# Performance work log

Hardware: AMD Instinct MI355X
Metric: run time of the kernel (lower is better)

Reference implementation:

```python
import jax, jax.numpy as jnp
import numpy as np

BS, N_STK, N_STK_PNT = 4, 32, 128
N_PNT = N_STK * N_STK_PNT
SP_IN, DN_IN = 128, 128
SP_OUT, DN_OUT = 256, 256
SP_NEAR, DN_NEAR = 2, 10
COOR = 128


def _conv2d(x, w, b, stride=(1, 1), pad='VALID'):
    # x [bs,C,H,W], w [O,I,kh,kw]
    y = jax.lax.conv_general_dilated(x, w, window_strides=stride, padding=pad,
                                     dimension_numbers=('NCHW', 'OIHW', 'NCHW'))
    return y + b[None, :, None, None]


def _fps(xyz, n_sample):
    # farthest point sampling. xyz [bs,n,c] -> [bs,n_sample] int32
    n = xyz.shape[1]

    def one(x):
        def body(i, state):
            idx, dist, far = state
            idx = idx.at[i].set(far)
            d = jnp.sum((x - x[far]) ** 2, axis=-1)
            dist = jnp.minimum(dist, d)
            return idx, dist, jnp.argmax(dist).astype(jnp.int32)

        idx0 = jnp.zeros((n_sample,), jnp.int32)
        dist0 = jnp.full((n,), 1e10, x.dtype)
        idx, _, _ = jax.lax.fori_loop(0, n_sample, body, (idx0, dist0, jnp.int32(0)))
        return idx

    return jax.vmap(one)(xyz)


def _gcn(x, W, b, g, bt, k):
    # DGCNN edge-conv. x [bs,c,n]; W [2c,co]
    xt = jnp.swapaxes(x, 1, 2)                                   # [bs,n,c]
    sq = jnp.sum(xt * xt, axis=-1)                               # [bs,n]
    dist = sq[:, :, None] - 2.0 * jnp.einsum('bnc,bmc->bnm', xt, xt) + sq[:, None, :]
    _, idx = jax.lax.top_k(-dist, k)                             # [bs,n,k]
    nbr = jax.vmap(lambda p, i: p[i])(xt, idx)                   # [bs,n,k,c]
    ctr = jnp.broadcast_to(xt[:, :, None, :], nbr.shape)
    edge = jnp.concatenate([ctr, nbr - ctr], axis=-1)            # [bs,n,k,2c]
    h = jnp.einsum('bnke,eo->bnko', edge, W) + b
    h = jax.nn.relu(g * h + bt)
    return jnp.swapaxes(jnp.max(h, axis=2), 1, 2)                # [bs,co,n]


def setup_inputs() -> dict:
    key = jax.random.key(0)
    ks = jax.random.split(key, 16)
    f32 = jnp.float32
    d = {
        'sparse_fea': jax.random.normal(ks[0], (BS, SP_IN, N_STK), f32),
        'dense_fea': jax.random.normal(ks[1], (BS, DN_IN, N_PNT), f32),
        'stk_coor': jax.random.normal(ks[2], (BS, N_STK, COOR), f32),
        # DenseToSparse: Conv2d(dn_in->dn_in, (1,3)) + BN
        'd2s_w': jax.random.normal(ks[3], (DN_IN, DN_IN, 1, 3), f32) * 0.05,
        'd2s_b': jnp.zeros((DN_IN,), f32),
        'd2s_g': jnp.ones((DN_IN,), f32),
        'd2s_bt': jnp.zeros((DN_IN,), f32),
        # sparse GCN: in = SP_IN + DN_IN, edge feat 2*in
        'sp_W': jax.random.normal(ks[4], (2 * (SP_IN + DN_IN), SP_OUT), f32) * 0.05,
        'sp_b': jnp.zeros((SP_OUT,), f32),
        'sp_g': jnp.ones((SP_OUT,), f32),
        'sp_bt': jnp.zeros((SP_OUT,), f32),
        # dense GCN: in = DN_IN + SP_IN
        'dn_W': jax.random.normal(ks[5], (2 * (DN_IN + SP_IN), DN_OUT), f32) * 0.05,
        'dn_b': jnp.zeros((DN_OUT,), f32),
        'dn_g': jnp.ones((DN_OUT,), f32),
        'dn_bt': jnp.zeros((DN_OUT,), f32),
        # DownSample: Conv2d(dn_out->dn_out, (1,3), stride (1,2), pad (0,1)) + BN
        'ds_w': jax.random.normal(ks[6], (DN_OUT, DN_OUT, 1, 3), f32) * 0.05,
        'ds_b': jnp.zeros((DN_OUT,), f32),
        'ds_g': jnp.ones((DN_OUT,), f32),
        'ds_bt': jnp.zeros((DN_OUT,), f32),
    }
    return d


def reference(sparse_fea, dense_fea, stk_coor,
              d2s_w, d2s_b, d2s_g, d2s_bt,
              sp_W, sp_b, sp_g, sp_bt,
              dn_W, dn_b, dn_g, dn_bt,
              ds_w, ds_b, ds_g, ds_bt):
    bs = sparse_fea.shape[0]
    df = dense_fea.reshape(bs, DN_IN, N_STK, N_STK_PNT)
    # DenseToSparse: conv (1,3) valid + BN(eval) + relu + max over stroke points
    h = _conv2d(df, d2s_w, d2s_b)
    h = jax.nn.relu(d2s_g[None, :, None, None] * h + d2s_bt[None, :, None, None])
    sp_from_dn = jnp.max(h, axis=3)                                    # [bs,dn_in,n_stk]
    union_sparse = jnp.concatenate([sparse_fea, sp_from_dn], axis=1)   # [bs,sp_in+dn_in,n_stk]
    # SparseToDense: broadcast stroke feature onto its points
    dn_from_sp = jnp.broadcast_to(sparse_fea[:, :, :, None], (bs, SP_IN, N_STK, N_STK_PNT))
    union_dense = jnp.concatenate([df, dn_from_sp], axis=1).reshape(bs, DN_IN + SP_IN, N_PNT)
    # GCN (DGCNN edge conv) updates
    sparse_up = _gcn(union_sparse, sp_W, sp_b, sp_g, sp_bt, SP_NEAR)   # [bs,SP_OUT,n_stk]
    dense_up = _gcn(union_dense, dn_W, dn_b, dn_g, dn_bt, DN_NEAR)     # [bs,DN_OUT,n_pnt]
    # DownSample: FPS on stroke coords, gather strokes, strided conv on points
    n_half = N_STK // 2
    fps_idx = _fps(stk_coor, n_half)                                   # [bs,n_half]
    stk_coor_s = jnp.take_along_axis(stk_coor, fps_idx[:, :, None], axis=1)
    sp_s = jnp.take_along_axis(jnp.swapaxes(sparse_up, 1, 2), fps_idx[:, :, None], axis=1)
    sp_s = jnp.swapaxes(sp_s, 1, 2)                                    # [bs,SP_OUT,n_half]
    dn = dense_up.reshape(bs, DN_OUT, N_STK, N_STK_PNT)
    dn = jnp.take_along_axis(dn, fps_idx[:, None, :, None], axis=2)    # [bs,DN_OUT,n_half,n_stk_pnt]
    dn = _conv2d(dn, ds_w, ds_b, stride=(1, 2), pad=[(0, 0), (1, 1)])
    dn = jax.nn.relu(ds_g[None, :, None, None] * dn + ds_bt[None, :, None, None])
    dn = dn.reshape(bs, DN_OUT, n_half * (N_STK_PNT // 2))
    return sp_s, dn, stk_coor_s
```

## Files before the change

kernel.cpp:

```cpp
#include <hip/hip_runtime.h>

#define NPNT 4096
#define NSTK 32

typedef _Float16 half8 __attribute__((ext_vector_type(8)));
typedef float f32x4 __attribute__((ext_vector_type(4)));
typedef unsigned long long u64;

static const size_t OFF_XT   = 0;
static const size_t OFF_P    = 4194304;
static const size_t OFF_Q    = 8388608;
static const size_t OFF_SQD  = 12582912;
static const size_t OFF_SPFD = 12599296;
static const size_t OFF_XS   = 12615680;
static const size_t OFF_PS   = 12648448;
static const size_t OFF_QS   = 12681216;
static const size_t OFF_WSP  = 12746752;
static const size_t OFF_KNN  = 13402112;
static const size_t OFF_IDXS = 13565952;
static const size_t OFF_FPS  = 13566208;
static const size_t OFF_SD   = 13566272;

__device__ __forceinline__ void insertK(u64 lk[10], u64 k) {
  if (k >= lk[9]) return;
  lk[9] = k;
#pragma unroll
  for (int j = 9; j > 0; j--) {
    u64 a = lk[j-1], b2 = lk[j];
    bool sw = b2 < a;
    lk[j-1] = sw ? b2 : a;
    lk[j]   = sw ? a : b2;
  }
}

#define CASK(a, b) { u64 _x = (a), _y = (b); bool _s = _y < _x; \
  (a) = _s ? _y : _x; (b) = _s ? _x : _y; }

__device__ __forceinline__ void merge10(u64 lk[10], const u64 b[10]) {
  u64 c[10];
#pragma unroll
  for (int i = 0; i < 10; i++) { u64 t = b[9 - i]; u64 a = lk[i]; c[i] = a < t ? a : t; }
  CASK(c[0], c[5]); CASK(c[1], c[6]); CASK(c[2], c[7]); CASK(c[3], c[8]); CASK(c[4], c[9]);
  CASK(c[0], c[1]); CASK(c[1], c[2]); CASK(c[2], c[3]); CASK(c[3], c[4]);
  CASK(c[0], c[1]); CASK(c[1], c[2]); CASK(c[2], c[3]);
  CASK(c[0], c[1]); CASK(c[1], c[2]);
  CASK(c[0], c[1]);
  CASK(c[5], c[6]); CASK(c[6], c[7]); CASK(c[7], c[8]); CASK(c[8], c[9]);
  CASK(c[5], c[6]); CASK(c[6], c[7]); CASK(c[7], c[8]);
  CASK(c[5], c[6]); CASK(c[6], c[7]);
  CASK(c[5], c[6]);
#pragma unroll
  for (int i = 0; i < 10; i++) lk[i] = c[i];
}

__global__ __launch_bounds__(256) void k_pre(
    const float* __restrict__ df, const float* __restrict__ sf,
    const float* __restrict__ coor, const float* __restrict__ dnW,
    const float* __restrict__ d2sw, const float* __restrict__ d2scb,
    const float* __restrict__ d2sg, const float* __restrict__ d2sbt,
    _Float16* __restrict__ XH, _Float16* __restrict__ XL, float* __restrict__ sqd,
    _Float16* __restrict__ WPh, _Float16* __restrict__ WPl,
    _Float16* __restrict__ WQh, _Float16* __restrict__ WQl,
    float* __restrict__ spfd, int* __restrict__ fpsidx, float* __restrict__ out2) {
  __shared__ __align__(16) char SMEM[46080];
  const int bid = blockIdx.x;
  const int t = threadIdx.x;

  if (bid < 4) {
    int b = bid;
    float (*X)[132] = (float (*)[132])SMEM;
    float* dist = (float*)(SMEM + 16896);
    int* far_s  = (int*)(SMEM + 17024);
    int* sel    = (int*)(SMEM + 17028);
    for (int idx = t; idx < 32 * 32; idx += 256) {
      int r = idx >> 5, q = idx & 31;
      *(float4*)&X[r][q * 4] = *(const float4*)&coor[((size_t)b * 32 + r) * 128 + q * 4];
    }
    if (t < 32) dist[t] = 1e10f;
    if (t == 0) *far_s = 0;
    __syncthreads();
    for (int it = 0; it < 16; it++) {
      int far = *far_s;
      if (t == 0) sel[it] = far;
      if (t < 32) {
        float d = 0.0f;
        for (int c = 0; c < 128; c++) { float dd = X[t][c] - X[far][c]; d = fmaf(dd, dd, d); }
        float dm = dist[t];
        dist[t] = d < dm ? d : dm;
      }
      __syncthreads();
      if (t == 0) {
        float best = -1.0f; int bi = 0;
        for (int m = 0; m < 32; m++) if (dist[m] > best) { best = dist[m]; bi = m; }
        *far_s = bi;
      }
      __syncthreads();
    }
    if (t < 16) fpsidx[b * 16 + t] = sel[t];
    __syncthreads();
    for (int idx = t; idx < 16 * 32; idx += 256) {
      int j = idx >> 5, q = idx & 31;
      *(float4*)&out2[((size_t)b * 16 + j) * 128 + q * 4] = *(const float4*)&X[sel[j]][q * 4];
    }
  } else if (bid < 260) {
    int idx0 = bid - 4;
    int b = idx0 & 3, n0 = (idx0 >> 2) * 64;
    int s0 = n0 >> 7;
    float (*T)[68] = (float (*)[68])SMEM;
    _Float16* Sh = (_Float16*)(SMEM + 34816);
    _Float16* Sl = (_Float16*)(SMEM + 35072);
    {
      int c = t >> 1, nh = (t & 1) * 32;
      const float* src = &df[((size_t)b * 128 + c) * NPNT + n0 + nh];
#pragma unroll
      for (int j = 0; j < 8; j++) *(float4*)&T[c][nh + j * 4] = *(const float4*)&src[j * 4];
    }
    if (t < 128) {
      float x = sf[((size_t)b * 128 + t) * NSTK + s0];
      _Float16 hi = (_Float16)x;
      Sh[t] = hi; Sl[t] = (_Float16)(x - (float)hi);
    }
    __syncthreads();
    {
      int n = t >> 2, cseg = (t & 3) * 32;
      size_t base = ((size_t)b * NPNT + n0 + n) * 256;
      float s = 0.0f;
#pragma unroll
      for (int k = 0; k < 4; k++) {
        half8 hv, lv, shv, slv;
#pragma unroll
        for (int e = 0; e < 8; e++) {
          float x = T[cseg + k * 8 + e][n];
          s = fmaf(x, x, s);
          _Float16 hi = (_Float16)x;
          hv[e] = hi; lv[e] = (_Float16)(x - (float)hi);
          shv[e] = Sh[cseg + k * 8 + e];
          slv[e] = Sl[cseg + k * 8 + e];
        }
        *(half8*)&XH[base + cseg + k * 8] = hv;
        *(half8*)&XL[base + cseg + k * 8] = lv;
        *(half8*)&XH[base + 128 + cseg + k * 8] = shv;
        *(half8*)&XL[base + 128 + cseg + k * 8] = slv;
      }
      s += __shfl_xor(s, 1);
      s += __shfl_xor(s, 2);
      if ((t & 3) == 0) sqd[(size_t)b * NPNT + n0 + n] = s;
    }
  } else if (bid < 516) {
    int idx0 = bid - 260;
    int b = idx0 & 3, o0 = ((idx0 >> 2) & 1) * 64, s = idx0 >> 3;
    int n0 = s * 128;
    float (*A)[64]   = (float (*)[64])SMEM;
    float (*Bs)[132] = (float (*)[132])(SMEM + 24576);
    float (*Dr)[17]  = (float (*)[17])(SMEM + 41472);
    float acc[4][8];
#pragma unroll
    for (int i = 0; i < 4; i++)
#pragma unroll
      for (int j = 0; j < 8; j++) acc[i][j] = 0.0f;
    int tn = t & 15, to = t >> 4;
    for (int ic = 0; ic < 128; ic += 32) {
      {
        int ol = t >> 2, q = t & 3;
        const float* src = &d2sw[((size_t)(o0 + ol) * 128 + ic) * 3 + q * 24];
#pragma unroll
        for (int r = 0; r < 6; r++) {
          float4 v = *(const float4*)&src[r * 4];
          int e = q * 24 + r * 4;
          A[e+0][ol] = v.x; A[e+1][ol] = v.y; A[e+2][ol] = v.z; A[e+3][ol] = v.w;
        }
      }
      for (int idx = t; idx < 32 * 33; idx += 256) {
        int row = idx / 33, f4 = idx % 33;
        int nb = n0 + f4 * 4;
        const float* srow = &df[((size_t)b * 128 + ic + row) * NPNT];
        float4 v;
        if (nb + 3 < NPNT) v = *(const float4*)&srow[nb];
        else {
          v.x = srow[nb   < NPNT ? nb   : NPNT-1];
          v.y = srow[nb+1 < NPNT ? nb+1 : NPNT-1];
          v.z = srow[nb+2 < NPNT ? nb+2 : NPNT-1];
          v.w = srow[nb+3 < NPNT ? nb+3 : NPNT-1];
        }
        *(float4*)&Bs[row][f4 * 4] = v;
      }
      __syncthreads();
#pragma unroll 2
      for (int ii = 0; ii < 32; ii++) {
        float bv[12];
        *(float4*)&bv[0] = *(const float4*)&Bs[ii][tn * 8];
        *(float4*)&bv[4] = *(const float4*)&Bs[ii][tn * 8 + 4];
        *(float4*)&bv[8] = *(const float4*)&Bs[ii][tn * 8 + 8];
#pragma unroll
        for (int kw = 0; kw < 3; kw++) {
          float4 av = *(const float4*)&A[ii * 3 + kw][to * 4];
#pragma unroll
          for (int j = 0; j < 8; j++) {
            float bvj = bv[kw + j];
            acc[0][j] = fmaf(av.x, bvj, acc[0][j]);
            acc[1][j] = fmaf(av.y, bvj, acc[1][j]);
            acc[2][j] = fmaf(av.z, bvj, acc[2][j]);
            acc[3][j] = fmaf(av.w, bvj, acc[3][j]);
          }
        }
      }
      __syncthreads();
    }
#pragma unroll
    for (int i = 0; i < 4; i++) {
      int o = o0 + to * 4 + i;
      float gg = d2sg[o], bb = d2scb[o], bo = d2sbt[o];
      float m = 0.0f;
#pragma unroll
      for (int j = 0; j < 8; j++) {
        int p = tn * 8 + j;
        if (p < 126) {
          float v = fmaf(gg, acc[i][j] + bb, bo);
          v = v > 0.0f ? v : 0.0f;
          m = v > m ? v : m;
        }
      }
      Dr[to * 4 + i][tn] = m;
    }
    __syncthreads();
    if (t < 64) {
      float m = 0.0f;
#pragma unroll
      for (int k = 0; k < 16; k++) m = Dr[t][k] > m ? Dr[t][k] : m;
      spfd[((size_t)b * 128 + o0 + t) * NSTK + s] = m;
    }
  } else {
    int k = bid - 516, o = t;
    float w1 = dnW[(size_t)k * 256 + o];
    float w2 = dnW[(size_t)(k + 256) * 256 + o];
    float p = w1 - w2;
    _Float16 ph = (_Float16)p;  WPh[(size_t)o * 256 + k] = ph;
    WPl[(size_t)o * 256 + k] = (_Float16)(p - (float)ph);
    _Float16 qh = (_Float16)w2; WQh[(size_t)o * 256 + k] = qh;
    WQl[(size_t)o * 256 + k] = (_Float16)(w2 - (float)qh);
  }
}

__global__ __launch_bounds__(256) void k_sparse_graph(const float* __restrict__ sf, const float* __restrict__ spfd,
    float* __restrict__ xs, int* __restrict__ idxs, float* __restrict__ SD) {
  int b = blockIdx.x, t = threadIdx.x;
  __shared__ float X[32][260];
  __shared__ float sq[32];
  __shared__ float D[32][33];
  for (int idx = t; idx < 32 * 256; idx += 256) {
    int n = idx >> 8, c = idx & 255;
    float v = (c < 128) ? sf[((size_t)b * 128 + c) * NSTK + n]
                        : spfd[((size_t)b * 128 + (c - 128)) * NSTK + n];
    X[n][c] = v;
  }
  __syncthreads();
  for (int idx = t; idx < 32 * 64; idx += 256) {
    int n = idx >> 6, q = idx & 63;
    *(float4*)&xs[((size_t)b * 32 + n) * 256 + q * 4] = *(const float4*)&X[n][q * 4];
  }
#pragma unroll
  for (int rep = 0; rep < 4; rep++) {
    int p = t + rep * 256;
    int s = p >> 5, u = p & 31;
    float acc = 0.0f;
    for (int c = 0; c < 128; c++) {
      float d = X[s][c] - X[u][c];
      acc = fmaf(d, d, acc);
    }
    SD[(size_t)b * 1024 + p] = acc;
  }
  if (t < 32) {
    float s = 0.0f;
    for (int c = 0; c < 256; c++) s = fmaf(X[t][c], X[t][c], s);
    sq[t] = s;
  }
  __syncthreads();
  {
    int n = t >> 3;
    for (int mg = 0; mg < 4; mg++) {
      int m = (t & 7) + mg * 8;
      float dot = 0.0f;
      for (int c = 0; c < 256; c++) dot = fmaf(X[n][c], X[m][c], dot);
      D[n][m] = (sq[n] - 2.0f * dot) + sq[m];
    }
  }
  __syncthreads();
  if (t < 32) {
    float d0 = 1e30f, d1 = 1e30f; int i0 = 0, i1 = 0;
    for (int m = 0; m < 32; m++) {
      float d = D[t][m];
      if (d < d0) { d1 = d0; i1 = i0; d0 = d; i0 = m; }
      else if (d < d1) { d1 = d; i1 = m; }
    }
    idxs[(b * 32 + t) * 2 + 0] = i0;
    idxs[(b * 32 + t) * 2 + 1] = i1;
  }
}

__global__ __launch_bounds__(256) void k_sparse_pq(const float* __restrict__ xs, const float* __restrict__ W,
    float* __restrict__ Ps, float* __restrict__ Qs) {
  int b = blockIdx.x >> 5, n = blockIdx.x & 31;
  int o = threadIdx.x;
  const float* xr = &xs[((size_t)b * 32 + n) * 256];
  float accP = 0.0f, accQ = 0.0f;
  for (int c = 0; c < 256; c++) {
    float xc = xr[c];
    float w1 = W[(size_t)c * 256 + o];
    float w2 = W[(size_t)(c + 256) * 256 + o];
    accP = fmaf(xc, w1 - w2, accP);
    accQ = fmaf(xc, w2, accQ);
  }
  Ps[((size_t)b * 32 + n) * 256 + o] = accP;
  Qs[((size_t)b * 32 + n) * 256 + o] = accQ;
}

__global__ __launch_bounds__(256) void k_sparse_cg(const float* __restrict__ Ps, const float* __restrict__ Qs,
    const int* __restrict__ idxs, const int* __restrict__ fps,
    const float* __restrict__ g, const float* __restrict__ cb, const float* __restrict__ bt,
    float* __restrict__ out0) {
  int b = blockIdx.x, j = blockIdx.y, o = threadIdx.x;
  int n = fps[b * 16 + j];
  int i0 = idxs[(b * 32 + n) * 2 + 0], i1 = idxs[(b * 32 + n) * 2 + 1];
  float p = Ps[((size_t)b * 32 + n) * 256 + o];
  float q0 = Qs[((size_t)b * 32 + i0) * 256 + o];
  float q1 = Qs[((size_t)b * 32 + i1) * 256 + o];
  float gg = g[o], bb = cb[o], bo = bt[o];
  float h0 = fmaf(gg, p + q0 + bb, bo); h0 = h0 > 0.0f ? h0 : 0.0f;
  float h1 = fmaf(gg, p + q1 + bb, bo); h1 = h1 > 0.0f ? h1 : 0.0f;
  out0[((size_t)b * 256 + o) * 16 + j] = h0 > h1 ? h0 : h1;
}

#define STAGE(ch2_, p_) { \
  int srow = t >> 2, scol = (t & 3) * 16; \
  size_t gp = (bofs + (size_t)(m0 + (ch2_) * 64 + srow)) * 256 + (p_) * 64 + scol; \
  float4 gh0 = *(const float4*)&XH[gp]; float4 gh1 = *(const float4*)&XH[gp + 8]; \
  float4 gl0 = *(const float4*)&XL[gp]; float4 gl1 = *(const float4*)&XL[gp + 8]; \
  int lo = srow * 72 + scol; \
  *(float4*)&BshH[lo] = gh0; *(float4*)&BshH[lo + 8] = gh1; \
  *(float4*)&BshL[lo] = gl0; *(float4*)&BshL[lo + 8] = gl1; }

#define DWU(wv_, r_, c_) DwU[(((wv_) * 16 + (r_)) * 68) + (c_)]

__global__ __launch_bounds__(256, 4) void k_knn_mfma(const _Float16* __restrict__ XH,
    const _Float16* __restrict__ XL, const float* __restrict__ sqd, const float* __restrict__ SD,
    const int* __restrict__ fps, u64* __restrict__ pk) {
  const int h = blockIdx.x, rb = blockIdx.y, b = blockIdx.z;
  const int t = threadIdx.x;
  const int w = t >> 6, L = t & 63;
  const int c15 = L & 15, q = L >> 4;
  const int jst = rb >> 1;
  const int ph = (rb & 1) * 64;
  const int s_stk = fps[b * 16 + jst];
  const int nsrc = s_stk * 128 + ph + w * 16;
  const int rc0 = rb * 64 + w * 16;
  const size_t bofs = (size_t)b * NPNT;

  __shared__ __align__(16) char SMEM[18432];
  _Float16* const BshH = (_Float16*)SMEM;
  _Float16* const BshL = (_Float16*)(SMEM + 64 * 72 * 2);
  unsigned* const DwU = (unsigned*)SMEM;

  half8 ah[4], al[4];
  {
    const _Float16* ap  = XH + (bofs + nsrc + c15) * 256 + q * 8;
    const _Float16* apl = XL + (bofs + nsrc + c15) * 256 + q * 8;
#pragma unroll
    for (int ch = 0; ch < 4; ch++) {
      ah[ch] = *(const half8*)(ap + ch * 32);
      al[ch] = *(const half8*)(apl + ch * 32);
    }
  }
  float snr[4];
#pragma unroll
  for (int r = 0; r < 4; r++) snr[r] = sqd[bofs + nsrc + q * 4 + r];

  u64 lk[10];
#pragma unroll
  for (int j = 0; j < 10; j++) lk[j] = ~0ull;

  const bool own_here = ((s_stk >> 1) == h);
  const int r_sel = L >> 2, sl = L & 3;
  const int u0 = own_here ? s_stk : (h * 2);
  const int u1 = own_here ? (s_stk ^ 1) : (h * 2 + 1);

#pragma unroll 1
  for (int it = 0; it < 2; it++) {
    const int u = (it == 0) ? u0 : u1;
    const int m0 = u * 128;
    const float SDv = SD[((size_t)b * 32 + s_stk) * 32 + u];

#pragma unroll 1
    for (int ch2 = 0; ch2 < 2; ch2++) {
      float smv[4];
#pragma unroll
      for (int cg = 0; cg < 4; cg++) smv[cg] = sqd[bofs + m0 + ch2 * 64 + cg * 16 + c15];

      f32x4 zz = {0.0f, 0.0f, 0.0f, 0.0f};
      f32x4 acc[4];
#pragma unroll
      for (int cg = 0; cg < 4; cg++) acc[cg] = zz;

      __syncthreads();
      STAGE(ch2, 0);
      __syncthreads();
#pragma unroll
      for (int chl = 0; chl < 2; chl++) {
#pragma unroll
        for (int cg = 0; cg < 4; cg++) {
          int lo = (cg * 16 + c15) * 72 + chl * 32 + q * 8;
          half8 bh = *(const half8*)&BshH[lo];
          half8 bl = *(const half8*)&BshL[lo];
          acc[cg] = __builtin_amdgcn_mfma_f32_16x16x32_f16(ah[chl], bh, acc[cg], 0, 0, 0);
          acc[cg] = __builtin_amdgcn_mfma_f32_16x16x32_f16(ah[chl], bl, acc[cg], 0, 0, 0);
          acc[cg] = __builtin_amdgcn_mfma_f32_16x16x32_f16(al[chl], bh, acc[cg], 0, 0, 0);
        }
      }
      __syncthreads();
      STAGE(ch2, 1);
      __syncthreads();
#pragma unroll
      for (int chl = 0; chl < 2; chl++) {
#pragma unroll
        for (int cg = 0; cg < 4; cg++) {
          int lo = (cg * 16 + c15) * 72 + chl * 32 + q * 8;
          half8 bh = *(const half8*)&BshH[lo];
          half8 bl = *(const half8*)&BshL[lo];
          acc[cg] = __builtin_amdgcn_mfma_f32_16x16x32_f16(ah[2 + chl], bh, acc[cg], 0, 0, 0);
          acc[cg] = __builtin_amdgcn_mfma_f32_16x16x32_f16(ah[2 + chl], bl, acc[cg], 0, 0, 0);
          acc[cg] = __builtin_amdgcn_mfma_f32_16x16x32_f16(al[2 + chl], bh, acc[cg], 0, 0, 0);
        }
      }
      __syncthreads();

#pragma unroll
      for (int cg = 0; cg < 4; cg++) {
        float basec = SDv + smv[cg];
#pragma unroll
        for (int r = 0; r < 4; r++) {
          float d = fmaf(-2.0f, acc[cg][r], snr[r] + basec);
          unsigned uu = __float_as_uint(d);
          unsigned kk = uu ^ ((unsigned)((int)uu >> 31) | 0x80000000u);
          DWU(w, q * 4 + r, cg * 16 + c15) = kk;
        }
      }
#pragma unroll
      for (int jj = 0; jj < 4; jj++) {
        uint4 kv = *(const uint4*)&DWU(w, r_sel, jj * 16 + sl * 4);
        int ib = m0 + ch2 * 64 + jj * 16 + sl * 4;
        insertK(lk, ((u64)kv.x << 32) | (unsigned)(ib + 0));
        insertK(lk, ((u64)kv.y << 32) | (unsigned)(ib + 1));
        insertK(lk, ((u64)kv.z << 32) | (unsigned)(ib + 2));
        insertK(lk, ((u64)kv.w << 32) | (unsigned)(ib + 3));
      }
    }
  }

#pragma unroll
  for (int m = 1; m <= 2; m <<= 1) {
    u64 o[10];
#pragma unroll
    for (int j = 0; j < 10; j++) o[j] = __shfl_xor(lk[j], m);
    merge10(lk, o);
  }
  if (sl == 0) {
    size_t row = (size_t)b * 2048 + rc0 + r_sel;
    u64* dst = &pk[(row * 16 + h) * 10];
#pragma unroll
    for (int j = 0; j < 10; j++) dst[j] = lk[j];
  }
}

__global__ __launch_bounds__(256) void k_knn_merge(const u64* __restrict__ pk,
                                                   int* __restrict__ knnc) {
  int gid = blockIdx.x * 256 + threadIdx.x;
  size_t row = (size_t)(gid >> 2);
  int sl = gid & 3;
  const u64* src = &pk[row * 160 + (size_t)sl * 40];
  u64 lk[10];
#pragma unroll
  for (int j = 0; j < 10; j++) lk[j] = src[j];
#pragma unroll
  for (int l = 1; l < 4; l++) {
    u64 bv[10];
#pragma unroll
    for (int j = 0; j < 10; j++) bv[j] = src[l * 10 + j];
    merge10(lk, bv);
  }
#pragma unroll
  for (int m = 1; m <= 2; m <<= 1) {
    u64 o[10];
#pragma unroll
    for (int j = 0; j < 10; j++) o[j] = __shfl_xor(lk[j], m);
    merge10(lk, o);
  }
  if (sl == 0) {
#pragma unroll
    for (int j = 0; j < 10; j++) knnc[row * 10 + j] = (int)(unsigned)(lk[j] & 0xffffffffull);
  }
}

__global__ __launch_bounds__(256, 2) void k_pq_mfma(const _Float16* __restrict__ XH, const _Float16* __restrict__ XL,
    const _Float16* __restrict__ WPh, const _Float16* __restrict__ WPl,
    const _Float16* __restrict__ WQh, const _Float16* __restrict__ WQl,
    const int* __restrict__ fps, const float* __restrict__ g, const float* __restrict__ cb,
    const float* __restrict__ bt, float* __restrict__ Pc, float* __restrict__ Qp) {
  const int b = blockIdx.z;
  const int t = threadIdx.x, w = t >> 6, L = t & 63;
  const int c15 = L & 15, q = L >> 4;
  const int ow = blockIdx.y * 128 + (w >> 1) * 64;
  const size_t bofs = (size_t)b * NPNT;
  f32x4 zz = {0.0f, 0.0f, 0.0f, 0.0f};

  {
    const int nw = blockIdx.x * 32 + (w & 1) * 16;
    f32x4 accQ[4];
#pragma unroll
    for (int cg = 0; cg < 4; cg++) accQ[cg] = zz;
    const _Float16* ap  = XH + (bofs + nw + c15) * 256 + q * 8;
    const _Float16* apl = XL + (bofs + nw + c15) * 256 + q * 8;
#pragma unroll
    for (int ch = 0; ch < 8; ch++) {
      half8 a_h = *(const half8*)(ap + ch * 32);
      half8 a_l = *(const half8*)(apl + ch * 32);
#pragma unroll
      for (int cg = 0; cg < 4; cg++) {
        size_t wb = (size_t)(ow + cg * 16 + c15) * 256 + ch * 32 + q * 8;
        half8 bqh = *(const half8*)(WQh + wb);
        half8 bql = *(const half8*)(WQl + wb);
        accQ[cg] = __builtin_amdgcn_mfma_f32_16x16x32_f16(a_h, bqh, accQ[cg], 0, 0, 0);
        accQ[cg] = __builtin_amdgcn_mfma_f32_16x16x32_f16(a_h, bql, accQ[cg], 0, 0, 0);
        accQ[cg] = __builtin_amdgcn_mfma_f32_16x16x32_f16(a_l, bqh, accQ[cg], 0, 0, 0);
      }
    }
#pragma unroll
    for (int cg = 0; cg < 4; cg++) {
      int o = ow + cg * 16 + c15;
      float gg = g[o];
#pragma unroll
      for (int r = 0; r < 4; r++) {
        Qp[(bofs + nw + q * 4 + r) * 256 + o] = gg * accQ[cg][r];
      }
    }
  }

  if (blockIdx.x < 64) {
    const int m0 = blockIdx.x * 32 + (w & 1) * 16;
    const int jst = m0 >> 7;
    const int pbase = m0 & 127;
    const int nsrc = fps[b * 16 + jst] * 128 + pbase;
    f32x4 accP[4];
#pragma unroll
    for (int cg = 0; cg < 4; cg++) accP[cg] = zz;
    const _Float16* ap  = XH + (bofs + nsrc + c15) * 256 + q * 8;
    const _Float16* apl = XL + (bofs + nsrc + c15) * 256 + q * 8;
#pragma unroll
    for (int ch = 0; ch < 8; ch++) {
      half8 a_h = *(const half8*)(ap + ch * 32);
      half8 a_l = *(const half8*)(apl + ch * 32);
#pragma unroll
      for (int cg = 0; cg < 4; cg++) {
        size_t wb = (size_t)(ow + cg * 16 + c15) * 256 + ch * 32 + q * 8;
        half8 bph = *(const half8*)(WPh + wb);
        half8 bpl = *(const half8*)(WPl + wb);
        accP[cg] = __builtin_amdgcn_mfma_f32_16x16x32_f16(a_h, bph, accP[cg], 0, 0, 0);
        accP[cg] = __builtin_amdgcn_mfma_f32_16x16x32_f16(a_h, bpl, accP[cg], 0, 0, 0);
        accP[cg] = __builtin_amdgcn_mfma_f32_16x16x32_f16(a_l, bph, accP[cg], 0, 0, 0);
      }
    }
#pragma unroll
    for (int cg = 0; cg < 4; cg++) {
      int o = ow + cg * 16 + c15;
      float gg = g[o], bb = cb[o], bo = bt[o];
#pragma unroll
      for (int r = 0; r < 4; r++) {
        Pc[(((size_t)b * 16 + jst) * 128 + pbase + q * 4 + r) * 256 + o] =
            fmaf(gg, accP[cg][r] + bb, bo);
      }
    }
  }
}

__global__ __launch_bounds__(256) void k_build_E(const float* __restrict__ Pc, const float* __restrict__ Qp,
    const int* __restrict__ knnc, float* __restrict__ E) {
  int pp = blockIdx.x, j = blockIdx.y, b = blockIdx.z;
  int t = threadIdx.x;
  float v[3];
#pragma unroll
  for (int dp = 0; dp < 3; dp++) {
    int p = 2 * pp - 1 + dp;
    float val = 0.0f;
    if (p >= 0 && p < 128) {
      size_t m = ((size_t)b * 16 + j) * 128 + p;
      float pv = Pc[m * 256 + t];
      const int* id = &knnc[m * 10];
      float mx = 0.0f;
#pragma unroll
      for (int k = 0; k < 10; k++) {
        float qv = Qp[((size_t)b * NPNT + id[k]) * 256 + t];
        float h = pv + qv;
        mx = h > mx ? h : mx;
      }
      val = mx;
    }
    v[dp] = val;
  }
  size_t base = ((size_t)(b * 16 + j) * 64 + pp) * 768;
  E[base + 3 * t + 0] = v[0];
  E[base + 3 * t + 1] = v[1];
  E[base + 3 * t + 2] = v[2];
}

__global__ __launch_bounds__(256) void k_ds_gemm(const float* __restrict__ Wd, const float* __restrict__ E,
    const float* __restrict__ cb, const float* __restrict__ g, const float* __restrict__ bt,
    float* __restrict__ out1) {
  int j0 = blockIdx.x * 64, o0 = blockIdx.y * 64, b = blockIdx.z;
  int t = threadIdx.x;
  __shared__ float A[32][68];
  __shared__ float Bs[32][68];
  float acc[4][4];
#pragma unroll
  for (int i = 0; i < 4; i++)
#pragma unroll
    for (int j = 0; j < 4; j++) acc[i][j] = 0.0f;
  int tj = t & 15, to = t >> 4;
  for (int kc = 0; kc < 768; kc += 32) {
    {
      int ol = t >> 2, q = t & 3;
      const float* src = &Wd[(size_t)(o0 + ol) * 768 + kc + q * 8];
      float4 v0 = *(const float4*)src, v1 = *(const float4*)(src + 4);
      int cc = q * 8;
      A[cc+0][ol] = v0.x; A[cc+1][ol] = v0.y; A[cc+2][ol] = v0.z; A[cc+3][ol] = v0.w;
      A[cc+4][ol] = v1.x; A[cc+5][ol] = v1.y; A[cc+6][ol] = v1.z; A[cc+7][ol] = v1.w;
    }
    {
      int jl = t >> 2, q = t & 3;
      const float* src = &E[((size_t)b * 1024 + j0 + jl) * 768 + kc + q * 8];
      float4 v0 = *(const float4*)src, v1 = *(const float4*)(src + 4);
      int cc = q * 8;
      Bs[cc+0][jl] = v0.x; Bs[cc+1][jl] = v0.y; Bs[cc+2][jl] = v0.z; Bs[cc+3][jl] = v0.w;
      Bs[cc+4][jl] = v1.x; Bs[cc+5][jl] = v1.y; Bs[cc+6][jl] = v1.z; Bs[cc+7][jl] = v1.w;
    }
    __syncthreads();
#pragma unroll 4
    for (int k = 0; k < 32; k++) {
      float4 a = *(const float4*)&A[k][to * 4];
      float4 bv = *(const float4*)&Bs[k][tj * 4];
      float av[4] = {a.x, a.y, a.z, a.w};
      float bb[4] = {bv.x, bv.y, bv.z, bv.w};
#pragma unroll
      for (int i = 0; i < 4; i++)
#pragma unroll
        for (int j = 0; j < 4; j++)
          acc[i][j] = fmaf(av[i], bb[j], acc[i][j]);
    }
    __syncthreads();
  }
#pragma unroll
  for (int i = 0; i < 4; i++) {
    int o = o0 + to * 4 + i;
    float gg = g[o], bb = cb[o], bo = bt[o];
    float4 v;
    float x0 = fmaf(gg, acc[i][0] + bb, bo); v.x = x0 > 0.0f ? x0 : 0.0f;
    float x1 = fmaf(gg, acc[i][1] + bb, bo); v.y = x1 > 0.0f ? x1 : 0.0f;
    float x2 = fmaf(gg, acc[i][2] + bb, bo); v.z = x2 > 0.0f ? x2 : 0.0f;
    float x3 = fmaf(gg, acc[i][3] + bb, bo); v.w = x3 > 0.0f ? x3 : 0.0f;
    *(float4*)&out1[((size_t)b * 256 + o) * 1024 + j0 + tj * 4] = v;
  }
}

extern "C" void kernel_launch(void* const* d_in, const int* in_sizes, int n_in,
                              void* d_out, int out_size, void* d_ws, size_t ws_size,
                              hipStream_t stream) {
  (void)in_sizes; (void)n_in; (void)out_size; (void)ws_size;
  const float* sf    = (const float*)d_in[0];
  const float* df    = (const float*)d_in[1];
  const float* coor  = (const float*)d_in[2];
  const float* d2sw  = (const float*)d_in[3];
  const float* d2sb  = (const float*)d_in[4];
  const float* d2sg  = (const float*)d_in[5];
  const float* d2sbt = (const float*)d_in[6];
  const float* spW   = (const float*)d_in[7];
  const float* spb   = (const float*)d_in[8];
  const float* spg   = (const float*)d_in[9];
  const float* spbt  = (const float*)d_in[10];
  const float* dnW   = (const float*)d_in[11];
  const float* dnb   = (const float*)d_in[12];
  const float* dng   = (const float*)d_in[13];
  const float* dnbt  = (const float*)d_in[14];
  const float* dsw   = (const float*)d_in[15];
  const float* dsb   = (const float*)d_in[16];
  const float* dsg   = (const float*)d_in[17];
  const float* dsbt  = (const float*)d_in[18];

  float* ws   = (float*)d_ws;
  float* Pc   = ws + OFF_P;
  float* Qp   = ws + OFF_Q;
  float* SQD  = ws + OFF_SQD;
  float* SPFD = ws + OFF_SPFD;
  float* XS   = ws + OFF_XS;
  float* PS   = ws + OFF_PS;
  float* QS   = ws + OFF_QS;
  int*   KNNC = (int*)(ws + OFF_KNN);
  int*   IDXS = (int*)(ws + OFF_IDXS);
  int*   FPS  = (int*)(ws + OFF_FPS);
  float* SD   = ws + OFF_SD;
  _Float16* XT2H = (_Float16*)(ws + OFF_XT);
  _Float16* XT2L = XT2H + (size_t)4 * NPNT * 256;
  float* E = ws + OFF_XT;
  _Float16* WPh = (_Float16*)(ws + OFF_WSP);
  _Float16* WPl = WPh + 65536;
  _Float16* WQh = WPh + 131072;
  _Float16* WQl = WPh + 196608;
  u64* PK = (u64*)(ws + OFF_Q);

  float* out0 = (float*)d_out;
  float* out1 = out0 + 16384;
  float* out2 = out1 + 1048576;

  k_pre<<<dim3(772), 256, 0, stream>>>(df, sf, coor, dnW, d2sw, d2sb, d2sg, d2sbt,
                                       XT2H, XT2L, SQD, WPh, WPl, WQh, WQl,
                                       SPFD, FPS, out2);
  k_sparse_graph<<<dim3(4), 256, 0, stream>>>(sf, SPFD, XS, IDXS, SD);
  k_sparse_pq<<<dim3(128), 256, 0, stream>>>(XS, spW, PS, QS);
  k_sparse_cg<<<dim3(4, 16), 256, 0, stream>>>(PS, QS, IDXS, FPS, spg, spb, spbt, out0);
  k_knn_mfma<<<dim3(16, 32, 4), 256, 0, stream>>>(XT2H, XT2L, SQD, SD, FPS, PK);
  k_knn_merge<<<dim3(128), 256, 0, stream>>>(PK, KNNC);
  k_pq_mfma<<<dim3(128, 2, 4), 256, 0, stream>>>(XT2H, XT2L, WPh, WPl, WQh, WQl,
                                                 FPS, dng, dnb, dnbt, Pc, Qp);
  k_build_E<<<dim3(64, 16, 4), 256, 0, stream>>>(Pc, Qp, KNNC, E);
  k_ds_gemm<<<dim3(16, 4, 4), 256, 0, stream>>>(dsw, E, dsb, dsg, dsbt, out1);
}
```

Before: 411.9 us.

## Replace im2col E buffer with per-point max buffer and implicit im2col in GEMM

Instead of materialising a 3x-expanded im2col tensor E (each point's neighbour max recomputed up to three times), the max over neighbours is computed once per point into buffer M. The downsample GEMM then gathers the three kernel taps from M directly, and the conv weights are pre-permuted in k_pre so that K is ordered tap-major. This removes redundant gathers and memory traffic in the build step. The k_pq_mfma launch bound also rises to 4 blocks per SM, which may force register spills.

Measured after the change: 417.2 us. About the same (+1.3%).

```diff
diff --git a/kernel.cpp b/kernel.cpp
--- a/kernel.cpp
+++ b/kernel.cpp
@@ -58,9 +58,11 @@
     const float* __restrict__ coor, const float* __restrict__ dnW,
     const float* __restrict__ d2sw, const float* __restrict__ d2scb,
     const float* __restrict__ d2sg, const float* __restrict__ d2sbt,
+    const float* __restrict__ dsw,
     _Float16* __restrict__ XH, _Float16* __restrict__ XL, float* __restrict__ sqd,
     _Float16* __restrict__ WPh, _Float16* __restrict__ WPl,
     _Float16* __restrict__ WQh, _Float16* __restrict__ WQl,
+    float* __restrict__ WDP,
     float* __restrict__ spfd, int* __restrict__ fpsidx, float* __restrict__ out2) {
   __shared__ __align__(16) char SMEM[46080];
   const int bid = blockIdx.x;
@@ -229,7 +231,7 @@
       for (int k = 0; k < 16; k++) m = Dr[t][k] > m ? Dr[t][k] : m;
       spfd[((size_t)b * 128 + o0 + t) * NSTK + s] = m;
     }
-  } else {
+  } else if (bid < 772) {
     int k = bid - 516, o = t;
     float w1 = dnW[(size_t)k * 256 + o];
     float w2 = dnW[(size_t)(k + 256) * 256 + o];
@@ -238,6 +240,13 @@
     WPl[(size_t)o * 256 + k] = (_Float16)(p - (float)ph);
     _Float16 qh = (_Float16)w2; WQh[(size_t)o * 256 + k] = qh;
     WQl[(size_t)o * 256 + k] = (_Float16)(w2 - (float)qh);
+  } else {
+    int o = bid - 772;
+    const float* src = &dsw[(size_t)o * 768];
+    float* dst = &WDP[(size_t)o * 768];
+#pragma unroll
+    for (int kw = 0; kw < 3; kw++)
+      dst[kw * 256 + t] = src[t * 3 + kw];
   }
 }
 
@@ -499,7 +508,7 @@
   }
 }
 
-__global__ __launch_bounds__(256, 2) void k_pq_mfma(const _Float16* __restrict__ XH, const _Float16* __restrict__ XL,
+__global__ __launch_bounds__(256, 4) void k_pq_mfma(const _Float16* __restrict__ XH, const _Float16* __restrict__ XL,
     const _Float16* __restrict__ WPh, const _Float16* __restrict__ WPl,
     const _Float16* __restrict__ WQh, const _Float16* __restrict__ WQl,
     const int* __restrict__ fps, const float* __restrict__ g, const float* __restrict__ cb,
@@ -580,40 +589,32 @@
   }
 }
 
-__global__ __launch_bounds__(256) void k_build_E(const float* __restrict__ Pc, const float* __restrict__ Qp,
-    const int* __restrict__ knnc, float* __restrict__ E) {
-  int pp = blockIdx.x, j = blockIdx.y, b = blockIdx.z;
+__global__ __launch_bounds__(256) void k_build_M(const float* __restrict__ Pc, const float* __restrict__ Qp,
+    const int* __restrict__ knnc, float* __restrict__ M) {
+  int pc = blockIdx.x, j = blockIdx.y, b = blockIdx.z;
   int t = threadIdx.x;
-  float v[3];
-#pragma unroll
-  for (int dp = 0; dp < 3; dp++) {
-    int p = 2 * pp - 1 + dp;
-    float val = 0.0f;
-    if (p >= 0 && p < 128) {
-      size_t m = ((size_t)b * 16 + j) * 128 + p;
-      float pv = Pc[m * 256 + t];
-      const int* id = &knnc[m * 10];
-      float mx = 0.0f;
-#pragma unroll
-      for (int k = 0; k < 10; k++) {
-        float qv = Qp[((size_t)b * NPNT + id[k]) * 256 + t];
-        float h = pv + qv;
-        mx = h > mx ? h : mx;
-      }
-      val = mx;
-    }
-    v[dp] = val;
-  }
-  size_t base = ((size_t)(b * 16 + j) * 64 + pp) * 768;
-  E[base + 3 * t + 0] = v[0];
-  E[base + 3 * t + 1] = v[1];
-  E[base + 3 * t + 2] = v[2];
-}
-
-__global__ __launch_bounds__(256) void k_ds_gemm(const float* __restrict__ Wd, const float* __restrict__ E,
+  int p0 = pc * 16;
+#pragma unroll 1
+  for (int pi = 0; pi < 16; pi++) {
+    size_t m = ((size_t)b * 16 + j) * 128 + p0 + pi;
+    float pv = Pc[m * 256 + t];
+    const int* id = &knnc[m * 10];
+    float mx = 0.0f;
+#pragma unroll
+    for (int k = 0; k < 10; k++) {
+      float qv = Qp[((size_t)b * NPNT + id[k]) * 256 + t];
+      float h = pv + qv;
+      mx = h > mx ? h : mx;
+    }
+    M[m * 256 + t] = mx;
+  }
+}
+
+__global__ __launch_bounds__(256) void k_ds_gemm(const float* __restrict__ WDP, const float* __restrict__ M,
     const float* __restrict__ cb, const float* __restrict__ g, const float* __restrict__ bt,
     float* __restrict__ out1) {
-  int j0 = blockIdx.x * 64, o0 = blockIdx.y * 64, b = blockIdx.z;
+  int j = blockIdx.x, o0 = blockIdx.y * 64, b = blockIdx.z;
+  int j0 = j * 64;
   int t = threadIdx.x;
   __shared__ float A[32][68];
   __shared__ float Bs[32][68];
@@ -621,12 +622,12 @@
 #pragma unroll
   for (int i = 0; i < 4; i++)
 #pragma unroll
-    for (int j = 0; j < 4; j++) acc[i][j] = 0.0f;
+    for (int jj = 0; jj < 4; jj++) acc[i][jj] = 0.0f;
   int tj = t & 15, to = t >> 4;
   for (int kc = 0; kc < 768; kc += 32) {
     {
       int ol = t >> 2, q = t & 3;
-      const float* src = &Wd[(size_t)(o0 + ol) * 768 + kc + q * 8];
+      const float* src = &WDP[(size_t)(o0 + ol) * 768 + kc + q * 8];
       float4 v0 = *(const float4*)src, v1 = *(const float4*)(src + 4);
       int cc = q * 8;
       A[cc+0][ol] = v0.x; A[cc+1][ol] = v0.y; A[cc+2][ol] = v0.z; A[cc+3][ol] = v0.w;
@@ -634,8 +635,15 @@
     }
     {
       int jl = t >> 2, q = t & 3;
-      const float* src = &E[((size_t)b * 1024 + j0 + jl) * 768 + kc + q * 8];
-      float4 v0 = *(const float4*)src, v1 = *(const float4*)(src + 4);
+      int kw = kc >> 8, cbl = (kc & 255) + q * 8;
+      int p = 2 * jl - 1 + kw;
+      float4 v0, v1;
+      if (p >= 0) {
+        const float* src = &M[(((size_t)b * 16 + j) * 128 + p) * 256 + cbl];
+        v0 = *(const float4*)src; v1 = *(const float4*)(src + 4);
+      } else {
+        v0.x = v0.y = v0.z = v0.w = 0.0f; v1 = v0;
+      }
       int cc = q * 8;
       Bs[cc+0][jl] = v0.x; Bs[cc+1][jl] = v0.y; Bs[cc+2][jl] = v0.z; Bs[cc+3][jl] = v0.w;
       Bs[cc+4][jl] = v1.x; Bs[cc+5][jl] = v1.y; Bs[cc+6][jl] = v1.z; Bs[cc+7][jl] = v1.w;
@@ -650,8 +658,8 @@
 #pragma unroll
       for (int i = 0; i < 4; i++)
 #pragma unroll
-        for (int j = 0; j < 4; j++)
-          acc[i][j] = fmaf(av[i], bb[j], acc[i][j]);
+        for (int jj = 0; jj < 4; jj++)
+          acc[i][jj] = fmaf(av[i], bb[jj], acc[i][jj]);
     }
     __syncthreads();
   }
@@ -706,20 +714,21 @@
   float* SD   = ws + OFF_SD;
   _Float16* XT2H = (_Float16*)(ws + OFF_XT);
   _Float16* XT2L = XT2H + (size_t)4 * NPNT * 256;
-  float* E = ws + OFF_XT;
+  float* Mb = ws + OFF_XT;
   _Float16* WPh = (_Float16*)(ws + OFF_WSP);
   _Float16* WPl = WPh + 65536;
   _Float16* WQh = WPh + 131072;
   _Float16* WQl = WPh + 196608;
+  float* WDP = ws + OFF_WSP + 131072;
   u64* PK = (u64*)(ws + OFF_Q);
 
   float* out0 = (float*)d_out;
   float* out1 = out0 + 16384;
   float* out2 = out1 + 1048576;
 
-  k_pre<<<dim3(772), 256, 0, stream>>>(df, sf, coor, dnW, d2sw, d2sb, d2sg, d2sbt,
-                                       XT2H, XT2L, SQD, WPh, WPl, WQh, WQl,
-                                       SPFD, FPS, out2);
+  k_pre<<<dim3(1028), 256, 0, stream>>>(df, sf, coor, dnW, d2sw, d2sb, d2sg, d2sbt, dsw,
+                                        XT2H, XT2L, SQD, WPh, WPl, WQh, WQl, WDP,
+                                        SPFD, FPS, out2);
   k_sparse_graph<<<dim3(4), 256, 0, stream>>>(sf, SPFD, XS, IDXS, SD);
   k_sparse_pq<<<dim3(128), 256, 0, stream>>>(XS, spW, PS, QS);
   k_sparse_cg<<<dim3(4, 16), 256, 0, stream>>>(PS, QS, IDXS, FPS, spg, spb, spbt, out0);
@@ -727,6 +736,6 @@
   k_knn_merge<<<dim3(128), 256, 0, stream>>>(PK, KNNC);
   k_pq_mfma<<<dim3(128, 2, 4), 256, 0, stream>>>(XT2H, XT2L, WPh, WPl, WQh, WQl,
                                                  FPS, dng, dnb, dnbt, Pc, Qp);
-  k_build_E<<<dim3(64, 16, 4), 256, 0, stream>>>(Pc, Qp, KNNC, E);
-  k_ds_gemm<<<dim3(16, 4, 4), 256, 0, stream>>>(dsw, E, dsb, dsg, dsbt, out1);
-}
+  k_build_M<<<dim3(8, 16, 4), 256, 0, stream>>>(Pc, Qp, KNNC, Mb);
+  k_ds_gemm<<<dim3(16, 4, 4), 256, 0, stream>>>(WDP, Mb, dsb, dsg, dsbt, out1);
+}
```
